# Kernel tuning notes

Hardware: AMD Instinct MI355X
Metric: run time of the kernel (lower is better)

Reference implementation:

```python
import jax, jax.numpy as jnp
import numpy as np

B, D, H, W, N, R, K = 8, 192, 64, 64, 16, 6, 4
L = H * W
EPS = 1e-5


def setup_inputs() -> dict:
    key = jax.random.key(0)
    ks = jax.random.split(key, 6)
    return {
        "x": jax.random.normal(ks[0], (B, D, H, W), jnp.float32),
        "x_proj_weight": jax.random.normal(ks[1], (K, R + 2 * N, D), jnp.float32) * 0.05,
        "dt_projs_weight": jax.random.normal(ks[2], (K, D, R), jnp.float32) * 0.1,
        "dt_projs_bias": jax.random.normal(ks[3], (K, D), jnp.float32) * 0.1,
        "A_logs": jax.random.uniform(ks[4], (K * D, N), jnp.float32),  # A = -exp(A_logs) in (-e,-1)
        "Ds": jax.random.uniform(ks[5], (K * D,), jnp.float32),
        "norm_weight": jnp.ones((D,), jnp.float32),
        "norm_bias": jnp.zeros((D,), jnp.float32),
    }


def cross_scan(x):
    # x: [B,D,H,W] -> xs: [B,K=4,D,L]
    b, d, h, w = x.shape
    x0 = x.reshape(b, d, h * w)                      # row-major scan
    x1 = x.transpose(0, 1, 3, 2).reshape(b, d, h * w)  # column-major scan
    return jnp.stack([x0, x1, x0[..., ::-1], x1[..., ::-1]], axis=1)


def cross_merge(ys, h, w):
    # ys: [B,K=4,D,L] -> y: [B,D,L]
    b, k, d, l = ys.shape
    y01 = ys[:, 0] + ys[:, 2, :, ::-1]
    y23 = ys[:, 1] + ys[:, 3, :, ::-1]
    # undo the transpose of the column-major scan
    y23 = y23.reshape(b, d, w, h).transpose(0, 1, 3, 2).reshape(b, d, l)
    return y01 + y23


def selective_scan(u, dt, A, Bs, Cs, Dskip, dt_bias):
    # u, dt: [B,K,D,L]; A: [K,D,N]; Bs, Cs: [B,K,N,L]; Dskip, dt_bias: [K,D]
    dt = jax.nn.softplus(dt + dt_bias[None, :, :, None])
    dBu = dt * u
    # L-first for scan
    dt_l = dt.transpose(3, 0, 1, 2)    # [L,B,K,D]
    dBu_l = dBu.transpose(3, 0, 1, 2)  # [L,B,K,D]
    Bs_l = Bs.transpose(3, 0, 1, 2)    # [L,B,K,N]
    Cs_l = Cs.transpose(3, 0, 1, 2)    # [L,B,K,N]

    def step(h, inp):
        dt_t, dBu_t, B_t, C_t = inp
        dA = jnp.exp(dt_t[..., None] * A)                     # [B,K,D,N]
        h = h * dA + dBu_t[..., None] * B_t[:, :, None, :]    # [B,K,D,N]
        y = jnp.einsum('bkdn,bkn->bkd', h, C_t)
        return h, y

    h0 = jnp.zeros((u.shape[0], K, D, N), u.dtype)
    _, ys = jax.lax.scan(step, h0, (dt_l, dBu_l, Bs_l, Cs_l))
    ys = ys.transpose(1, 2, 3, 0)                             # [B,K,D,L]
    return ys + Dskip[None, :, :, None] * u


def reference(x, x_proj_weight, dt_projs_weight, dt_projs_bias, A_logs, Ds, norm_weight, norm_bias):
    b, d, h, w = x.shape
    l = h * w
    xs = cross_scan(x)                                        # [B,K,D,L]
    x_dbl = jnp.einsum('bkdl,kcd->bkcl', xs, x_proj_weight)   # [B,K,R+2N,L]
    dts, Bs, Cs = jnp.split(x_dbl, [R, R + N], axis=2)        # [B,K,R,L],[B,K,N,L],[B,K,N,L]
    dts = jnp.einsum('bkrl,kdr->bkdl', dts, dt_projs_weight)  # [B,K,D,L]
    A = -jnp.exp(A_logs).reshape(K, d, N)
    ys = selective_scan(xs, dts, A, Bs, Cs, Ds.reshape(K, d), dt_projs_bias)
    y = cross_merge(ys, h, w)                                 # [B,D,L]
    # out_norm (LayerNorm over channel dim, v0 path)
    y = y.transpose(0, 2, 1)                                  # [B,L,D]
    mu = jnp.mean(y, axis=-1, keepdims=True)
    var = jnp.mean(jnp.square(y - mu), axis=-1, keepdims=True)
    y = (y - mu) * jax.lax.rsqrt(var + EPS) * norm_weight + norm_bias
    return y.reshape(b, h, w, d).astype(x.dtype)
```

## Files before the change

kernel.cpp:

```cpp
#include <hip/hip_runtime.h>
#include <hip/hip_bf16.h>

#define LL 4096
#define DD 192
#define NN 16
#define NCH 64
#define LC  64

typedef float v2f __attribute__((ext_vector_type(2)));

__device__ __forceinline__ v2f v2(float a, float b) { v2f r; r.x = a; r.y = b; return r; }
__device__ __forceinline__ float fexp2(float x) { return __builtin_amdgcn_exp2f(x); }

__global__ __launch_bounds__(256) void k_proj(
    const float* __restrict__ x, const float* __restrict__ Wp,
    float* __restrict__ dtr, float* __restrict__ Bsv, float* __restrict__ Csv)
{
  const int tid = threadIdx.x;
  const int p = blockIdx.x * 256 + tid;
  const int k = blockIdx.y;
  const int b = blockIdx.z;
  const float* __restrict__ xrow = x + (size_t)b * DD * LL + p;

  float acc[38];
#pragma unroll
  for (int c = 0; c < 38; ++c) acc[c] = 0.f;

  const float* __restrict__ wk = Wp + k * 38 * DD;

  float xn0 = xrow[0 * LL], xn1 = xrow[1 * LL], xn2 = xrow[2 * LL], xn3 = xrow[3 * LL];
  for (int d0 = 0; d0 < DD; d0 += 4) {
    const float x0 = xn0, x1 = xn1, x2 = xn2, x3 = xn3;
    if (d0 + 4 < DD) {
      xn0 = xrow[(size_t)(d0 + 4) * LL];
      xn1 = xrow[(size_t)(d0 + 5) * LL];
      xn2 = xrow[(size_t)(d0 + 6) * LL];
      xn3 = xrow[(size_t)(d0 + 7) * LL];
    }
#pragma unroll
    for (int c = 0; c < 38; ++c) {
      const float* __restrict__ wr = wk + c * DD + d0;
      float a = acc[c];
      a = fmaf(x0, wr[0], a);
      a = fmaf(x1, wr[1], a);
      a = fmaf(x2, wr[2], a);
      a = fmaf(x3, wr[3], a);
      acc[c] = a;
    }
  }

  const int sp = ((p & 63) << 6) | (p >> 6);
  int ls;
  if      (k == 0) ls = p;
  else if (k == 1) ls = sp;
  else if (k == 2) ls = LL - 1 - p;
  else             ls = LL - 1 - sp;

  const size_t bk4 = (size_t)b * 4 + k;
  float* __restrict__ dr = dtr + (bk4 * LL + ls) * 8;
  *(float4*)(dr)     = make_float4(acc[0], acc[1], acc[2], acc[3]);
  *(float2*)(dr + 4) = make_float2(acc[4], acc[5]);
  float* __restrict__ br = Bsv + (bk4 * LL + ls) * NN;
  *(float4*)(br + 0)  = make_float4(acc[6],  acc[7],  acc[8],  acc[9]);
  *(float4*)(br + 4)  = make_float4(acc[10], acc[11], acc[12], acc[13]);
  *(float4*)(br + 8)  = make_float4(acc[14], acc[15], acc[16], acc[17]);
  *(float4*)(br + 12) = make_float4(acc[18], acc[19], acc[20], acc[21]);
  float* __restrict__ cr = Csv + (bk4 * LL + ls) * NN;
  *(float4*)(cr + 0)  = make_float4(acc[22], acc[23], acc[24], acc[25]);
  *(float4*)(cr + 4)  = make_float4(acc[26], acc[27], acc[28], acc[29]);
  *(float4*)(cr + 8)  = make_float4(acc[30], acc[31], acc[32], acc[33]);
  *(float4*)(cr + 12) = make_float4(acc[34], acc[35], acc[36], acc[37]);
}

__global__ __launch_bounds__(256) void k_xt(
    const float* __restrict__ x, __hip_bfloat16* __restrict__ xt)
{
  __shared__ float tile[64][65];
  const int b = blockIdx.z, d0 = blockIdx.y * 64, p0 = blockIdx.x * 64;
  const int tx = threadIdx.x & 63, ty = threadIdx.x >> 6;
#pragma unroll
  for (int r = ty; r < 64; r += 4)
    tile[r][tx] = x[((size_t)b * DD + d0 + r) * LL + p0 + tx];
  __syncthreads();
#pragma unroll
  for (int pr = ty; pr < 64; pr += 4)
    xt[((size_t)b * LL + p0 + pr) * DD + d0 + tx] = __float2bfloat16(tile[tx][pr]);
}

__device__ __forceinline__ int urow(int l, bool rev, bool trans) {
  const int rl = rev ? (LL - 1 - l) : l;
  return trans ? (((rl & 63) << 6) | (rl >> 6)) : rl;
}

__global__ __launch_bounds__(192) void k_partial(
    const float* __restrict__ dtr, const float* __restrict__ Bsv,
    const __hip_bfloat16* __restrict__ xt,
    const float* __restrict__ dtw, const float* __restrict__ dtb,
    const float* __restrict__ Alog,
    __hip_bfloat16* __restrict__ Pv, __hip_bfloat16* __restrict__ qv)
{
  const int d  = threadIdx.x;
  const int bk = blockIdx.x;
  const int c  = blockIdx.y;
  const int k = bk & 3, b = bk >> 2;
  const int kd = k * DD + d;
  const bool rev = (k >= 2), trans = (k & 1);
  const float L2E = 1.4426950408889634f;

  v2f An2[8];
#pragma unroll
  for (int j = 0; j < 8; ++j)
    An2[j] = v2(-__expf(Alog[(size_t)kd * NN + 2*j])     * L2E,
                -__expf(Alog[(size_t)kd * NN + 2*j + 1]) * L2E);
  const float w0 = dtw[kd*6+0], w1 = dtw[kd*6+1], w2 = dtw[kd*6+2],
              w3 = dtw[kd*6+3], w4 = dtw[kd*6+4], w5 = dtw[kd*6+5];
  const float bias = dtb[kd];
  const __hip_bfloat16* __restrict__ ub = xt + (size_t)b * LL * DD + d;
  const float* __restrict__ dtrp = dtr + (size_t)bk * LL * 8;
  const float* __restrict__ Bp   = Bsv + (size_t)bk * LL * NN;

  v2f P2[8], q2[8];
#pragma unroll
  for (int j = 0; j < 8; ++j) { P2[j] = v2(1.f, 1.f); q2[j] = v2(0.f, 0.f); }

  const int l0 = c * LC;
  float uc = __bfloat162float(ub[(size_t)urow(l0, rev, trans) * DD]);

#pragma unroll 2
  for (int i = 0; i < LC; ++i) {
    const int l = l0 + i;
    float un = 0.f;
    if (i + 1 < LC)
      un = __bfloat162float(ub[(size_t)urow(l + 1, rev, trans) * DD]);
    const float4 r0 = *(const float4*)(dtrp + (size_t)l * 8);
    const float2 r1 = *(const float2*)(dtrp + (size_t)l * 8 + 4);
    const float4 B0 = *(const float4*)(Bp + (size_t)l * NN);
    const float4 B1 = *(const float4*)(Bp + (size_t)l * NN + 4);
    const float4 B2 = *(const float4*)(Bp + (size_t)l * NN + 8);
    const float4 B3 = *(const float4*)(Bp + (size_t)l * NN + 12);
    float v = bias + r0.x*w0 + r0.y*w1 + r0.z*w2 + r0.w*w3 + r1.x*w4 + r1.y*w5;
    const float sp = (v > 20.f) ? v : __logf(1.f + __expf(v));
    const float dbu = sp * uc;
    const v2f sp2  = v2(sp, sp);
    const v2f dbu2 = v2(dbu, dbu);
    const v2f Bv[8] = { v2(B0.x,B0.y), v2(B0.z,B0.w), v2(B1.x,B1.y), v2(B1.z,B1.w),
                        v2(B2.x,B2.y), v2(B2.z,B2.w), v2(B3.x,B3.y), v2(B3.z,B3.w) };
#pragma unroll
    for (int j = 0; j < 8; ++j) {
      const v2f a = sp2 * An2[j];
      v2f e; e.x = fexp2(a.x); e.y = fexp2(a.y);
      P2[j] = P2[j] * e;
      q2[j] = __builtin_elementwise_fma(q2[j], e, dbu2 * Bv[j]);
    }
    uc = un;
  }

  __hip_bfloat16* __restrict__ Pp = Pv + (((size_t)bk * NCH + c) * DD + d) * NN;
  __hip_bfloat16* __restrict__ qp = qv + (((size_t)bk * NCH + c) * DD + d) * NN;
#pragma unroll
  for (int j = 0; j < 8; ++j) {
    Pp[2*j]   = __float2bfloat16(P2[j].x);
    Pp[2*j+1] = __float2bfloat16(P2[j].y);
    qp[2*j]   = __float2bfloat16(q2[j].x);
    qp[2*j+1] = __float2bfloat16(q2[j].y);
  }
}

__global__ __launch_bounds__(256) void k_comb(
    __hip_bfloat16* __restrict__ Pv, const __hip_bfloat16* __restrict__ qv)
{
  const int idx = blockIdx.x * 256 + threadIdx.x;
  const int dn = idx % (DD * NN);
  const int bk = idx / (DD * NN);
  const size_t base = (size_t)bk * NCH * DD * NN + dn;
  float h = 0.f;
  for (int c = 0; c < NCH; ++c) {
    const size_t a = base + (size_t)c * DD * NN;
    const float Pc = __bfloat162float(Pv[a]);
    const float qc = __bfloat162float(qv[a]);
    Pv[a] = __float2bfloat16(h);
    h = fmaf(Pc, h, qc);
  }
}

__global__ __launch_bounds__(192) void k_scanc(
    const float* __restrict__ dtr, const float* __restrict__ Bsv,
    const float* __restrict__ Csv, const __hip_bfloat16* __restrict__ xt,
    const float* __restrict__ dtw, const float* __restrict__ dtb,
    const float* __restrict__ Alog, const __hip_bfloat16* __restrict__ hin,
    __hip_bfloat16* __restrict__ ys)
{
  const int d  = threadIdx.x;
  const int bk = blockIdx.x;
  const int c  = blockIdx.y;
  const int k = bk & 3, b = bk >> 2;
  const int kd = k * DD + d;
  const bool rev = (k >= 2), trans = (k & 1);
  const float L2E = 1.4426950408889634f;

  v2f An2[8];
#pragma unroll
  for (int j = 0; j < 8; ++j)
    An2[j] = v2(-__expf(Alog[(size_t)kd * NN + 2*j])     * L2E,
                -__expf(Alog[(size_t)kd * NN + 2*j + 1]) * L2E);
  const float w0 = dtw[kd*6+0], w1 = dtw[kd*6+1], w2 = dtw[kd*6+2],
              w3 = dtw[kd*6+3], w4 = dtw[kd*6+4], w5 = dtw[kd*6+5];
  const float bias = dtb[kd];
  const __hip_bfloat16* __restrict__ ub = xt + (size_t)b * LL * DD + d;
  const float* __restrict__ dtrp = dtr + (size_t)bk * LL * 8;
  const float* __restrict__ Bp   = Bsv + (size_t)bk * LL * NN;
  const float* __restrict__ Cp   = Csv + (size_t)bk * LL * NN;
  __hip_bfloat16* __restrict__ yp = ys + (size_t)bk * LL * DD + d;

  v2f h2[8];
  const __hip_bfloat16* __restrict__ hp = hin + (((size_t)bk * NCH + c) * DD + d) * NN;
#pragma unroll
  for (int j = 0; j < 8; ++j)
    h2[j] = v2(__bfloat162float(hp[2*j]), __bfloat162float(hp[2*j+1]));

  const int l0 = c * LC;
  int rowc = urow(l0, rev, trans);
  float uc = __bfloat162float(ub[(size_t)rowc * DD]);

#pragma unroll 2
  for (int i = 0; i < LC; ++i) {
    const int l = l0 + i;
    int rown = 0; float un = 0.f;
    if (i + 1 < LC) {
      rown = urow(l + 1, rev, trans);
      un = __bfloat162float(ub[(size_t)rown * DD]);
    }
    const float4 r0 = *(const float4*)(dtrp + (size_t)l * 8);
    const float2 r1 = *(const float2*)(dtrp + (size_t)l * 8 + 4);
    const float4 B0 = *(const float4*)(Bp + (size_t)l * NN);
    const float4 B1 = *(const float4*)(Bp + (size_t)l * NN + 4);
    const float4 B2 = *(const float4*)(Bp + (size_t)l * NN + 8);
    const float4 B3 = *(const float4*)(Bp + (size_t)l * NN + 12);
    const float4 C0 = *(const float4*)(Cp + (size_t)l * NN);
    const float4 C1 = *(const float4*)(Cp + (size_t)l * NN + 4);
    const float4 C2 = *(const float4*)(Cp + (size_t)l * NN + 8);
    const float4 C3 = *(const float4*)(Cp + (size_t)l * NN + 12);
    float v = bias + r0.x*w0 + r0.y*w1 + r0.z*w2 + r0.w*w3 + r1.x*w4 + r1.y*w5;
    const float sp = (v > 20.f) ? v : __logf(1.f + __expf(v));
    const float dbu = sp * uc;
    const v2f sp2  = v2(sp, sp);
    const v2f dbu2 = v2(dbu, dbu);
    const v2f Bv[8] = { v2(B0.x,B0.y), v2(B0.z,B0.w), v2(B1.x,B1.y), v2(B1.z,B1.w),
                        v2(B2.x,B2.y), v2(B2.z,B2.w), v2(B3.x,B3.y), v2(B3.z,B3.w) };
    const v2f Cv[8] = { v2(C0.x,C0.y), v2(C0.z,C0.w), v2(C1.x,C1.y), v2(C1.z,C1.w),
                        v2(C2.x,C2.y), v2(C2.z,C2.w), v2(C3.x,C3.y), v2(C3.z,C3.w) };
    v2f ya = v2(0.f, 0.f), yb = v2(0.f, 0.f), yc = v2(0.f, 0.f), yd = v2(0.f, 0.f);
#pragma unroll
    for (int j = 0; j < 8; ++j) {
      const v2f a = sp2 * An2[j];
      v2f e; e.x = fexp2(a.x); e.y = fexp2(a.y);
      h2[j] = __builtin_elementwise_fma(h2[j], e, dbu2 * Bv[j]);
      v2f& yacc = (j < 2) ? ya : (j < 4) ? yb : (j < 6) ? yc : yd;
      yacc = __builtin_elementwise_fma(h2[j], Cv[j], yacc);
    }
    const v2f ysum = (ya + yb) + (yc + yd);
    yp[(size_t)rowc * DD] = __float2bfloat16(ysum.x + ysum.y);
    rowc = rown; uc = un;
  }
}

__global__ __launch_bounds__(64) void k_merge(
    const __hip_bfloat16* __restrict__ ys, const float* __restrict__ x,
    const float* __restrict__ Ds, const float* __restrict__ nw,
    const float* __restrict__ nb, float* __restrict__ out)
{
  const int lane = threadIdx.x;
  const int b = blockIdx.y;
  const int p0 = blockIdx.x * 16;

  float Dsum[3], nwv[3], nbv[3];
#pragma unroll
  for (int i = 0; i < 3; ++i) {
    int d = lane + 64 * i;
    Dsum[i] = Ds[d] + Ds[DD + d] + Ds[2 * DD + d] + Ds[3 * DD + d];
    nwv[i] = nw[d];
    nbv[i] = nb[d];
  }
  const __hip_bfloat16* __restrict__ ysb = ys + (size_t)b * 4 * LL * DD;
  const float* __restrict__ xb = x + (size_t)b * DD * LL;
  float* __restrict__ ob = out + (size_t)b * LL * DD;

  for (int chk = 0; chk < 2; ++chk) {
    const int q0 = p0 + chk * 8;
    float v[8][3];
    float xr[8][3];
#pragma unroll
    for (int i = 0; i < 3; ++i) {
      const float* __restrict__ xrow = xb + (size_t)(lane + 64 * i) * LL + q0;
      float4 x0 = *(const float4*)(xrow);
      float4 x1 = *(const float4*)(xrow + 4);
      xr[0][i]=x0.x; xr[1][i]=x0.y; xr[2][i]=x0.z; xr[3][i]=x0.w;
      xr[4][i]=x1.x; xr[5][i]=x1.y; xr[6][i]=x1.z; xr[7][i]=x1.w;
    }
#pragma unroll
    for (int j = 0; j < 8; ++j) {
      const int pos = q0 + j;
#pragma unroll
      for (int i = 0; i < 3; ++i) {
        const int d = lane + 64 * i;
        const size_t idx = (size_t)pos * DD + d;
        float s = __bfloat162float(ysb[idx])
                + __bfloat162float(ysb[(size_t)LL * DD + idx])
                + __bfloat162float(ysb[(size_t)2 * LL * DD + idx])
                + __bfloat162float(ysb[(size_t)3 * LL * DD + idx]);
        v[j][i] = s + xr[j][i] * Dsum[i];
      }
    }
#pragma unroll
    for (int j = 0; j < 8; ++j) {
      float s1 = v[j][0] + v[j][1] + v[j][2];
      float s2 = v[j][0]*v[j][0] + v[j][1]*v[j][1] + v[j][2]*v[j][2];
#pragma unroll
      for (int m = 1; m < 64; m <<= 1) {
        s1 += __shfl_xor(s1, m);
        s2 += __shfl_xor(s2, m);
      }
      const float mu  = s1 * (1.f / 192.f);
      const float var = s2 * (1.f / 192.f) - mu * mu;
      const float rs  = rsqrtf(var + 1e-5f);
      const int pos = q0 + j;
#pragma unroll
      for (int i = 0; i < 3; ++i) {
        ob[(size_t)pos * DD + lane + 64 * i] = (v[j][i] - mu) * rs * nwv[i] + nbv[i];
      }
    }
  }
}

extern "C" void kernel_launch(void* const* d_in, const int* in_sizes, int n_in,
                              void* d_out, int out_size, void* d_ws, size_t ws_size,
                              hipStream_t stream)
{
  (void)in_sizes; (void)n_in; (void)out_size; (void)ws_size;
  const float* x    = (const float*)d_in[0];
  const float* Wp   = (const float*)d_in[1];
  const float* dtw  = (const float*)d_in[2];
  const float* dtb  = (const float*)d_in[3];
  const float* Alog = (const float*)d_in[4];
  const float* Ds   = (const float*)d_in[5];
  const float* nw   = (const float*)d_in[6];
  const float* nb   = (const float*)d_in[7];
  float* out = (float*)d_out;
  float* ws  = (float*)d_ws;

  float* dtrw = ws;
  float* Bsv  = ws + 1048576;
  float* Csv  = ws + 3145728;
  __hip_bfloat16* xt  = (__hip_bfloat16*)(ws + 5242880);
  __hip_bfloat16* ysv = (__hip_bfloat16*)(ws + 8388608);
  __hip_bfloat16* Pv  = (__hip_bfloat16*)(ws + 20971520);
  __hip_bfloat16* qv  = (__hip_bfloat16*)(ws + 24117248);

  k_proj   <<<dim3(16, 4, 8), 256, 0, stream>>>(x, Wp, dtrw, Bsv, Csv);
  k_xt     <<<dim3(64, 3, 8), 256, 0, stream>>>(x, xt);
  k_partial<<<dim3(32, NCH), DD, 0, stream>>>(dtrw, Bsv, xt, dtw, dtb, Alog, Pv, qv);
  k_comb   <<<384, 256, 0, stream>>>(Pv, qv);
  k_scanc  <<<dim3(32, NCH), DD, 0, stream>>>(dtrw, Bsv, Csv, xt, dtw, dtb, Alog, Pv, ysv);
  k_merge  <<<dim3(256, 8), 64, 0, stream>>>(ysv, x, Ds, nw, nb, out);
}
```

Measured before the change: 398.2 us.

## Compute x projection with split-bf16 MFMA instead of scalar FP32 FMAs

Replaces the scalar FP32 projection kernel with an MFMA kernel that uses a hi/lo bf16 split (three MFMAs per tile) to keep close to FP32 accuracy. It reads the transposed bf16 copy of x that is already produced, adding a low-part copy, and uses weights repacked into a padded 48-row bf16 layout by a new small kernel. The goal is to cut the ALU-bound FMA cost of the projection, at the price of an extra kernel launch and more workspace traffic.

```diff
diff --git a/kernel.cpp b/kernel.cpp
--- a/kernel.cpp
+++ b/kernel.cpp
@@ -8,72 +8,31 @@
 #define LC  64
 
 typedef float v2f __attribute__((ext_vector_type(2)));
+typedef float f32x4 __attribute__((ext_vector_type(4)));
+typedef short bf16x8 __attribute__((ext_vector_type(8)));
 
 __device__ __forceinline__ v2f v2(float a, float b) { v2f r; r.x = a; r.y = b; return r; }
 __device__ __forceinline__ float fexp2(float x) { return __builtin_amdgcn_exp2f(x); }
 
-__global__ __launch_bounds__(256) void k_proj(
-    const float* __restrict__ x, const float* __restrict__ Wp,
-    float* __restrict__ dtr, float* __restrict__ Bsv, float* __restrict__ Csv)
-{
-  const int tid = threadIdx.x;
-  const int p = blockIdx.x * 256 + tid;
-  const int k = blockIdx.y;
-  const int b = blockIdx.z;
-  const float* __restrict__ xrow = x + (size_t)b * DD * LL + p;
-
-  float acc[38];
-#pragma unroll
-  for (int c = 0; c < 38; ++c) acc[c] = 0.f;
-
-  const float* __restrict__ wk = Wp + k * 38 * DD;
-
-  float xn0 = xrow[0 * LL], xn1 = xrow[1 * LL], xn2 = xrow[2 * LL], xn3 = xrow[3 * LL];
-  for (int d0 = 0; d0 < DD; d0 += 4) {
-    const float x0 = xn0, x1 = xn1, x2 = xn2, x3 = xn3;
-    if (d0 + 4 < DD) {
-      xn0 = xrow[(size_t)(d0 + 4) * LL];
-      xn1 = xrow[(size_t)(d0 + 5) * LL];
-      xn2 = xrow[(size_t)(d0 + 6) * LL];
-      xn3 = xrow[(size_t)(d0 + 7) * LL];
-    }
-#pragma unroll
-    for (int c = 0; c < 38; ++c) {
-      const float* __restrict__ wr = wk + c * DD + d0;
-      float a = acc[c];
-      a = fmaf(x0, wr[0], a);
-      a = fmaf(x1, wr[1], a);
-      a = fmaf(x2, wr[2], a);
-      a = fmaf(x3, wr[3], a);
-      acc[c] = a;
-    }
-  }
-
-  const int sp = ((p & 63) << 6) | (p >> 6);
-  int ls;
-  if      (k == 0) ls = p;
-  else if (k == 1) ls = sp;
-  else if (k == 2) ls = LL - 1 - p;
-  else             ls = LL - 1 - sp;
-
-  const size_t bk4 = (size_t)b * 4 + k;
-  float* __restrict__ dr = dtr + (bk4 * LL + ls) * 8;
-  *(float4*)(dr)     = make_float4(acc[0], acc[1], acc[2], acc[3]);
-  *(float2*)(dr + 4) = make_float2(acc[4], acc[5]);
-  float* __restrict__ br = Bsv + (bk4 * LL + ls) * NN;
-  *(float4*)(br + 0)  = make_float4(acc[6],  acc[7],  acc[8],  acc[9]);
-  *(float4*)(br + 4)  = make_float4(acc[10], acc[11], acc[12], acc[13]);
-  *(float4*)(br + 8)  = make_float4(acc[14], acc[15], acc[16], acc[17]);
-  *(float4*)(br + 12) = make_float4(acc[18], acc[19], acc[20], acc[21]);
-  float* __restrict__ cr = Csv + (bk4 * LL + ls) * NN;
-  *(float4*)(cr + 0)  = make_float4(acc[22], acc[23], acc[24], acc[25]);
-  *(float4*)(cr + 4)  = make_float4(acc[26], acc[27], acc[28], acc[29]);
-  *(float4*)(cr + 8)  = make_float4(acc[30], acc[31], acc[32], acc[33]);
-  *(float4*)(cr + 12) = make_float4(acc[34], acc[35], acc[36], acc[37]);
+__global__ __launch_bounds__(192) void k_wprep(
+    const float* __restrict__ Wp, __hip_bfloat16* __restrict__ Whi,
+    __hip_bfloat16* __restrict__ Wlo)
+{
+  const int d = threadIdx.x;
+  const int r = blockIdx.x;
+  const int k = r / 48, cc = r % 48;
+  float v = 0.f;
+  if      (cc < 6)               v = Wp[((size_t)k * 38 + cc) * DD + d];
+  else if (cc >= 8  && cc < 24)  v = Wp[((size_t)k * 38 + 6  + (cc - 8))  * DD + d];
+  else if (cc >= 24 && cc < 40)  v = Wp[((size_t)k * 38 + 22 + (cc - 24)) * DD + d];
+  const __hip_bfloat16 hi = __float2bfloat16(v);
+  Whi[(size_t)r * DD + d] = hi;
+  Wlo[(size_t)r * DD + d] = __float2bfloat16(v - __bfloat162float(hi));
 }
 
 __global__ __launch_bounds__(256) void k_xt(
-    const float* __restrict__ x, __hip_bfloat16* __restrict__ xt)
+    const float* __restrict__ x, __hip_bfloat16* __restrict__ xh,
+    __hip_bfloat16* __restrict__ xl)
 {
   __shared__ float tile[64][65];
   const int b = blockIdx.z, d0 = blockIdx.y * 64, p0 = blockIdx.x * 64;
@@ -83,8 +42,67 @@
     tile[r][tx] = x[((size_t)b * DD + d0 + r) * LL + p0 + tx];
   __syncthreads();
 #pragma unroll
-  for (int pr = ty; pr < 64; pr += 4)
-    xt[((size_t)b * LL + p0 + pr) * DD + d0 + tx] = __float2bfloat16(tile[tx][pr]);
+  for (int pr = ty; pr < 64; pr += 4) {
+    const float vv = tile[tx][pr];
+    const __hip_bfloat16 hi = __float2bfloat16(vv);
+    const size_t idx = ((size_t)b * LL + p0 + pr) * DD + d0 + tx;
+    xh[idx] = hi;
+    xl[idx] = __float2bfloat16(vv - __bfloat162float(hi));
+  }
+}
+
+__global__ __launch_bounds__(192) void k_mfproj(
+    const __hip_bfloat16* __restrict__ xh, const __hip_bfloat16* __restrict__ xl,
+    const __hip_bfloat16* __restrict__ Whi, const __hip_bfloat16* __restrict__ Wlo,
+    float* __restrict__ dtr, float* __restrict__ Bsv, float* __restrict__ Csv)
+{
+  const int tid  = threadIdx.x;
+  const int w    = tid >> 6;
+  const int lane = tid & 63;
+  const int n    = lane & 15;
+  const int quad = lane >> 4;
+  const int p0   = blockIdx.x * 16;
+  const int b    = blockIdx.y;
+  const int p    = p0 + n;
+
+  const short* __restrict__ xhp = (const short*)xh + ((size_t)b * LL + p) * DD + quad * 8;
+  const short* __restrict__ xlp = (const short*)xl + ((size_t)b * LL + p) * DD + quad * 8;
+  const short* __restrict__ whp = (const short*)Whi + ((size_t)(w * 4) * 16 + n) * DD + quad * 8;
+  const short* __restrict__ wlp = (const short*)Wlo + ((size_t)(w * 4) * 16 + n) * DD + quad * 8;
+
+  f32x4 acc[4];
+#pragma unroll
+  for (int m = 0; m < 4; ++m) acc[m] = (f32x4){0.f, 0.f, 0.f, 0.f};
+
+#pragma unroll
+  for (int ks = 0; ks < 6; ++ks) {
+    const bf16x8 bh = *(const bf16x8*)(xhp + ks * 32);
+    const bf16x8 bl = *(const bf16x8*)(xlp + ks * 32);
+#pragma unroll
+    for (int m = 0; m < 4; ++m) {
+      const bf16x8 ah = *(const bf16x8*)(whp + (size_t)m * 16 * DD + ks * 32);
+      const bf16x8 al = *(const bf16x8*)(wlp + (size_t)m * 16 * DD + ks * 32);
+      acc[m] = __builtin_amdgcn_mfma_f32_16x16x32_bf16(ah, bh, acc[m], 0, 0, 0);
+      acc[m] = __builtin_amdgcn_mfma_f32_16x16x32_bf16(ah, bl, acc[m], 0, 0, 0);
+      acc[m] = __builtin_amdgcn_mfma_f32_16x16x32_bf16(al, bh, acc[m], 0, 0, 0);
+    }
+  }
+
+  const int sg = ((p & 63) << 6) | (p >> 6);
+  int lsv[4] = { p, sg, LL - 1 - p, LL - 1 - sg };
+
+#pragma unroll
+  for (int m = 0; m < 4; ++m) {
+    const int mt = w * 4 + m;
+    const int k  = mt / 3;
+    const int t  = mt - k * 3;
+    const int cc0 = t * 16 + quad * 4;
+    const size_t rowb = (size_t)(b * 4 + k) * LL + lsv[k];
+    const float4 vv = make_float4(acc[m][0], acc[m][1], acc[m][2], acc[m][3]);
+    if      (cc0 < 8)  *(float4*)(dtr + rowb * 8  + cc0)        = vv;
+    else if (cc0 < 24) *(float4*)(Bsv + rowb * 16 + (cc0 - 8))  = vv;
+    else if (cc0 < 40) *(float4*)(Csv + rowb * 16 + (cc0 - 24)) = vv;
+  }
 }
 
 __device__ __forceinline__ int urow(int l, bool rev, bool trans) {
@@ -351,15 +369,19 @@
   float* dtrw = ws;
   float* Bsv  = ws + 1048576;
   float* Csv  = ws + 3145728;
-  __hip_bfloat16* xt  = (__hip_bfloat16*)(ws + 5242880);
+  __hip_bfloat16* xh  = (__hip_bfloat16*)(ws + 5242880);
   __hip_bfloat16* ysv = (__hip_bfloat16*)(ws + 8388608);
   __hip_bfloat16* Pv  = (__hip_bfloat16*)(ws + 20971520);
   __hip_bfloat16* qv  = (__hip_bfloat16*)(ws + 24117248);
-
-  k_proj   <<<dim3(16, 4, 8), 256, 0, stream>>>(x, Wp, dtrw, Bsv, Csv);
-  k_xt     <<<dim3(64, 3, 8), 256, 0, stream>>>(x, xt);
-  k_partial<<<dim3(32, NCH), DD, 0, stream>>>(dtrw, Bsv, xt, dtw, dtb, Alog, Pv, qv);
+  __hip_bfloat16* xlv = (__hip_bfloat16*)(ws + 27262976);
+  __hip_bfloat16* Whi = (__hip_bfloat16*)(ws + 30408704);
+  __hip_bfloat16* Wlo = (__hip_bfloat16*)(ws + 30427136);
+
+  k_wprep  <<<192, 192, 0, stream>>>(Wp, Whi, Wlo);
+  k_xt     <<<dim3(64, 3, 8), 256, 0, stream>>>(x, xh, xlv);
+  k_mfproj <<<dim3(256, 8), 192, 0, stream>>>(xh, xlv, Whi, Wlo, dtrw, Bsv, Csv);
+  k_partial<<<dim3(32, NCH), DD, 0, stream>>>(dtrw, Bsv, xh, dtw, dtb, Alog, Pv, qv);
   k_comb   <<<384, 256, 0, stream>>>(Pv, qv);
-  k_scanc  <<<dim3(32, NCH), DD, 0, stream>>>(dtrw, Bsv, Csv, xt, dtw, dtb, Alog, Pv, ysv);
+  k_scanc  <<<dim3(32, NCH), DD, 0, stream>>>(dtrw, Bsv, Csv, xh, dtw, dtb, Alog, Pv, ysv);
   k_merge  <<<dim3(256, 8), 64, 0, stream>>>(ysv, x, Ds, nw, nb, out);
 }
```

Result: faster. 367.8 us (-7.6%).
